# Kernel optimization log

Hardware: AMD Instinct MI355X
Metric: run time of the kernel (lower is better)

## Reference

```python
import jax, jax.numpy as jnp
import numpy as np

N = 16384          # total nodes (128 graphs x 128 ops)
G = 128            # number of graphs
NPG = N // G       # nodes per graph
DIN = 64           # op_input_dim
H = 64             # hidden_dim
BN_EPS = 1e-5


def setup_inputs() -> dict:
    key = jax.random.key(0)
    ks = jax.random.split(key, 16)
    x = jax.random.normal(ks[0], (N, DIN), dtype=jnp.float32)
    # sparse-ish 0/1 adjacency stored dense (as torch.mm path expects); add self-loops so degrees > 0
    u = jax.random.uniform(ks[1], (N, N), dtype=jnp.float32)
    adj = jnp.maximum((u < 0.004).astype(jnp.float32), jnp.eye(N, dtype=jnp.float32))
    # graph_pool: [G, N] average-pooling matrix (block rows of 1/NPG)
    rows = jnp.repeat(jnp.arange(G), NPG)
    graph_pool = jnp.zeros((G, N), jnp.float32).at[rows, jnp.arange(N)].set(1.0 / NPG)
    s = 0.05
    params = {}
    dims_in = [DIN, H]
    for l in range(2):
        d_in = dims_in[l]
        params[f"W1_{l}"] = jax.random.normal(ks[2 + 6 * l], (d_in, H), jnp.float32) * s
        params[f"b1_{l}"] = jnp.zeros((H,), jnp.float32)
        params[f"g1_{l}"] = jnp.ones((H,), jnp.float32)
        params[f"be1_{l}"] = jnp.zeros((H,), jnp.float32)
        params[f"W2_{l}"] = jax.random.normal(ks[3 + 6 * l], (H, H), jnp.float32) * s
        params[f"b2_{l}"] = jnp.zeros((H,), jnp.float32)
        params[f"g_{l}"] = jnp.ones((H,), jnp.float32)   # outer BN gamma
        params[f"be_{l}"] = jnp.zeros((H,), jnp.float32)  # outer BN beta
    return {"x": x, "adj": adj, "graph_pool": graph_pool, **params}


def _bn(h, g, b):
    # training-mode BatchNorm1d over node axis (biased var), eps=1e-5
    m = jnp.mean(h, axis=0)
    v = jnp.var(h, axis=0)
    return g * (h - m) * jax.lax.rsqrt(v + BN_EPS) + b


def _mlp(h, W1, b1, g1, be1, W2, b2):
    # 2-layer MLP: Linear -> BN -> ReLU -> Linear
    return jax.nn.relu(_bn(h @ W1 + b1, g1, be1)) @ W2 + b2


def reference(x, adj, graph_pool,
              W1_0, b1_0, g1_0, be1_0, W2_0, b2_0, g_0, be_0,
              W1_1, b1_1, g1_1, be1_1, W2_1, b2_1, g_1, be_1):
    deg = adj @ jnp.ones((adj.shape[0], 1), adj.dtype)  # [N,1]
    h = x
    layers = [
        (W1_0, b1_0, g1_0, be1_0, W2_0, b2_0, g_0, be_0),
        (W1_1, b1_1, g1_1, be1_1, W2_1, b2_1, g_1, be_1),
    ]
    for (W1, b1, g1, be1, W2, b2, g, be) in layers:
        pooled = (adj @ h) / deg                 # average neighbor aggregation
        pooled_rep = _mlp(pooled, W1, b1, g1, be1, W2, b2)
        h = jax.nn.relu(_bn(pooled_rep, g, be))
    h_nodes = h
    pooled_h = graph_pool @ h                    # [G, H] graph readout
    return (pooled_h, h_nodes)
```

## Files before the change

### kernel.cpp

```cpp
#include <hip/hip_runtime.h>
#include <hip/hip_bf16.h>
#include <stdint.h>

#define N_NODES 16384
#define GG      128
#define HD      64
#define MAXD    192
#define BN_EPS  1e-5f
#define NSLOT   16

typedef unsigned short u16;
typedef unsigned int   u32;
typedef unsigned long long u64;
typedef u32 u32x4 __attribute__((ext_vector_type(4)));

__device__ __forceinline__ float bf2f(u16 u) {
    union { u32 i; float f; } c; c.i = ((u32)u) << 16; return c.f;
}
__device__ __forceinline__ float ldp(const void* p, int i, int flag) {
    return flag ? ((const float*)p)[i] : bf2f(((const u16*)p)[i]);
}

__global__ __launch_bounds__(256) void k_scan_gather(
    const void* __restrict__ adjv, const void* __restrict__ xv,
    u16* __restrict__ cols, int* __restrict__ cnt,
    float* __restrict__ invdeg, float* __restrict__ pooled,
    double* __restrict__ statsD, int* __restrict__ flagp)
{
    __shared__ __align__(16) u16 sc[4][MAXD];
    const int wave = threadIdx.x >> 6, lane = threadIdx.x & 63;
    const int row = blockIdx.x * 4 + wave;
    const u32 w0 = *(const u32*)adjv;
    const int flag = ((w0 & 0xFFFFu) == 0) ? 1 : 0;
    const u64 ltmask = ((1ull << lane) - 1ull);

    const int gid = blockIdx.x * 256 + threadIdx.x;
    if (gid < 4 * NSLOT * 128) statsD[gid] = 0.0;
    if (gid == 0) *flagp = flag;

    u16* __restrict__ srow = sc[wave];
    int base = 0;
    if (flag) {
        const u32x4* __restrict__ arow =
            (const u32x4*)((const u32*)adjv + (size_t)row * N_NODES) + lane;
        u32x4 p0 = __builtin_nontemporal_load(arow);
        u32x4 p1 = __builtin_nontemporal_load(arow + 64);
        for (int c = 0; c < N_NODES; c += 256) {
            u32x4 raw = p0;
            p0 = p1;
            if (c + 512 < N_NODES)
                p1 = __builtin_nontemporal_load(arow + (c + 512) / 4);
            #pragma unroll
            for (int e = 0; e < 4; ++e) {
                u32 w = raw[e];
                u64 m = __ballot(w != 0);
                if (m) {
                    if (w) {
                        int p = base + __popcll(m & ltmask);
                        if (p < MAXD) srow[p] = (u16)(c + lane * 4 + e);
                    }
                    base += __popcll(m);
                }
            }
        }
    } else {
        const u32x4* __restrict__ arow =
            (const u32x4*)((const u16*)adjv + (size_t)row * N_NODES) + lane;
        u32x4 p0 = __builtin_nontemporal_load(arow);
        u32x4 p1 = __builtin_nontemporal_load(arow + 64);
        for (int c = 0; c < N_NODES; c += 512) {
            u32x4 raw = p0;
            p0 = p1;
            if (c + 1024 < N_NODES)
                p1 = __builtin_nontemporal_load(arow + (c + 1024) / 8);
            #pragma unroll
            for (int e = 0; e < 8; ++e) {
                u16 u = (u16)(raw[e >> 1] >> ((e & 1) * 16));
                u64 m = __ballot(u != 0);
                if (m) {
                    if (u) {
                        int p = base + __popcll(m & ltmask);
                        if (p < MAXD) srow[p] = (u16)(c + lane * 8 + e);
                    }
                    base += __popcll(m);
                }
            }
        }
    }
    const int n = (base < MAXD) ? base : MAXD;
    if (lane == 0) cnt[row] = n;
    __syncthreads();

    {
        u32* __restrict__ crow32 = (u32*)(cols + (size_t)row * MAXD);
        const u32* __restrict__ s32 = (const u32*)srow;
        #pragma unroll
        for (int t = lane; t < MAXD / 2; t += 64) crow32[t] = s32[t];
    }

    float acc = 0.f;
    int k = 0;
    if (flag) {
        const float* __restrict__ x = (const float*)xv;
        for (; k + 4 <= n; k += 4) {
            ushort4 j4 = *(const ushort4*)&srow[k];
            float v0 = x[(size_t)j4.x * HD + lane];
            float v1 = x[(size_t)j4.y * HD + lane];
            float v2 = x[(size_t)j4.z * HD + lane];
            float v3 = x[(size_t)j4.w * HD + lane];
            acc += (v0 + v1) + (v2 + v3);
        }
        for (; k < n; ++k) acc += x[(size_t)srow[k] * HD + lane];
    } else {
        const u16* __restrict__ x = (const u16*)xv;
        for (; k + 4 <= n; k += 4) {
            ushort4 j4 = *(const ushort4*)&srow[k];
            float v0 = bf2f(x[(size_t)j4.x * HD + lane]);
            float v1 = bf2f(x[(size_t)j4.y * HD + lane]);
            float v2 = bf2f(x[(size_t)j4.z * HD + lane]);
            float v3 = bf2f(x[(size_t)j4.w * HD + lane]);
            acc += (v0 + v1) + (v2 + v3);
        }
        for (; k < n; ++k) acc += bf2f(x[(size_t)srow[k] * HD + lane]);
    }
    float inv = 1.f / (float)n;
    pooled[(size_t)row * HD + lane] = acc * inv;
    if (lane == 0) invdeg[row] = inv;
}

template<bool AFFINE>
__global__ __launch_bounds__(256) void k_mm(
    const float* __restrict__ src, const double* __restrict__ statsIn,
    const void* __restrict__ g, const void* __restrict__ be,
    const void* __restrict__ W, const void* __restrict__ bias,
    float* __restrict__ dst, double* __restrict__ statsOut,
    const int* __restrict__ flagp)
{
    __shared__ float Wf[64 * 64];
    __shared__ float S[16 * 64];
    __shared__ float ac[128];
    __shared__ double shs[256];
    __shared__ double shq[256];
    const int tid = threadIdx.x;
    const int flag = *flagp;
    if (AFFINE) {
        if (tid < 64) {
            double ss = 0.0, qq = 0.0;
            #pragma unroll
            for (int s2 = 0; s2 < NSLOT; ++s2) {
                ss += statsIn[s2 * 128 + tid];
                qq += statsIn[s2 * 128 + 64 + tid];
            }
            double m = ss * (1.0 / N_NODES);
            double v = qq * (1.0 / N_NODES) - m * m;
            float A = ldp(g, tid, flag) / sqrtf((float)v + BN_EPS);
            ac[tid] = A;
            ac[64 + tid] = ldp(be, tid, flag) - (float)m * A;
        }
        __syncthreads();
    }
    for (int i = tid; i < 64 * 64; i += 256) Wf[i] = ldp(W, i, flag);
    const int rbase = blockIdx.x * 16;
    {
        float4 v = *(const float4*)&src[(size_t)rbase * 64 + tid * 4];
        if (AFFINE) {
            const int f0 = (tid * 4) & 63;
            v.x = fmaxf(fmaf(ac[f0 + 0], v.x, ac[64 + f0 + 0]), 0.f);
            v.y = fmaxf(fmaf(ac[f0 + 1], v.y, ac[64 + f0 + 1]), 0.f);
            v.z = fmaxf(fmaf(ac[f0 + 2], v.z, ac[64 + f0 + 2]), 0.f);
            v.w = fmaxf(fmaf(ac[f0 + 3], v.w, ac[64 + f0 + 3]), 0.f);
        }
        *(float4*)&S[tid * 4] = v;
    }
    __syncthreads();
    const int f = tid & 63, r0 = (tid >> 6) * 4;
    const float b = ldp(bias, f, flag);
    float a0 = b, a1 = b, a2 = b, a3 = b;
    #pragma unroll
    for (int k = 0; k < 64; ++k) {
        const float wk = Wf[k * 64 + f];
        a0 = fmaf(S[(r0 + 0) * 64 + k], wk, a0);
        a1 = fmaf(S[(r0 + 1) * 64 + k], wk, a1);
        a2 = fmaf(S[(r0 + 2) * 64 + k], wk, a2);
        a3 = fmaf(S[(r0 + 3) * 64 + k], wk, a3);
    }
    dst[(size_t)(rbase + r0 + 0) * 64 + f] = a0;
    dst[(size_t)(rbase + r0 + 1) * 64 + f] = a1;
    dst[(size_t)(rbase + r0 + 2) * 64 + f] = a2;
    dst[(size_t)(rbase + r0 + 3) * 64 + f] = a3;

    shs[tid] = (double)a0 + (double)a1 + (double)a2 + (double)a3;
    shq[tid] = (double)a0 * a0 + (double)a1 * a1
             + (double)a2 * a2 + (double)a3 * a3;
    __syncthreads();
    if (tid < 64) {
        double S2 = shs[tid] + shs[64 + tid] + shs[128 + tid] + shs[192 + tid];
        double Q2 = shq[tid] + shq[64 + tid] + shq[128 + tid] + shq[192 + tid];
        double* so = statsOut + (blockIdx.x & (NSLOT - 1)) * 128;
        atomicAdd(&so[tid], S2);
        atomicAdd(&so[64 + tid], Q2);
    }
}

__global__ __launch_bounds__(256) void k_spmm(
    const float* __restrict__ t, const double* __restrict__ statsIn,
    const void* __restrict__ g, const void* __restrict__ be,
    const u16* __restrict__ cols, const int* __restrict__ cnt,
    const float* __restrict__ invdeg, float* __restrict__ pooled,
    const int* __restrict__ flagp)
{
    __shared__ float ac[128];
    const int tid = threadIdx.x;
    const int wave = tid >> 6, lane = tid & 63;
    const int row = blockIdx.x * 4 + wave;
    const int flag = *flagp;
    if (tid < 64) {
        double ss = 0.0, qq = 0.0;
        #pragma unroll
        for (int s2 = 0; s2 < NSLOT; ++s2) {
            ss += statsIn[s2 * 128 + tid];
            qq += statsIn[s2 * 128 + 64 + tid];
        }
        double m = ss * (1.0 / N_NODES);
        double v = qq * (1.0 / N_NODES) - m * m;
        float A = ldp(g, tid, flag) / sqrtf((float)v + BN_EPS);
        ac[tid] = A;
        ac[64 + tid] = ldp(be, tid, flag) - (float)m * A;
    }
    __syncthreads();
    const float A = ac[lane], C = ac[64 + lane];

    const u16* __restrict__ crow = cols + (size_t)row * MAXD;
    const int n = cnt[row];
    float acc = 0.f;
    int k = 0;
    for (; k + 4 <= n; k += 4) {
        ushort4 j4 = *(const ushort4*)&crow[k];
        float v0 = t[(size_t)j4.x * HD + lane];
        float v1 = t[(size_t)j4.y * HD + lane];
        float v2 = t[(size_t)j4.z * HD + lane];
        float v3 = t[(size_t)j4.w * HD + lane];
        acc += fmaxf(fmaf(A, v0, C), 0.f);
        acc += fmaxf(fmaf(A, v1, C), 0.f);
        acc += fmaxf(fmaf(A, v2, C), 0.f);
        acc += fmaxf(fmaf(A, v3, C), 0.f);
    }
    for (; k < n; ++k) {
        float vv = t[(size_t)crow[k] * HD + lane];
        acc += fmaxf(fmaf(A, vv, C), 0.f);
    }
    pooled[(size_t)row * HD + lane] = acc * invdeg[row];
}

__global__ __launch_bounds__(1024) void k_bnrelu_pool(
    const float* __restrict__ P, const double* __restrict__ statsIn,
    const void* __restrict__ g, const void* __restrict__ be,
    const void* __restrict__ gpv, float* __restrict__ out_nodes,
    float* __restrict__ out_pool, const int* __restrict__ flagp)
{
    __shared__ float ac[128];
    __shared__ float red[16 * 64];
    const int tid = threadIdx.x;
    const int flag = *flagp;
    if (tid < 64) {
        double ss = 0.0, qq = 0.0;
        #pragma unroll
        for (int s2 = 0; s2 < NSLOT; ++s2) {
            ss += statsIn[s2 * 128 + tid];
            qq += statsIn[s2 * 128 + 64 + tid];
        }
        double m = ss * (1.0 / N_NODES);
        double v = qq * (1.0 / N_NODES) - m * m;
        float A = ldp(g, tid, flag) / sqrtf((float)v + BN_EPS);
        ac[tid] = A;
        ac[64 + tid] = ldp(be, tid, flag) - (float)m * A;
    }
    __syncthreads();

    if (blockIdx.x < 256) {
        const size_t idx = ((size_t)blockIdx.x * 1024 + tid) * 4;
        const int f0 = (int)(idx & 63);
        float4 t = *(const float4*)&P[idx];
        const float4 A4 = *(const float4*)&ac[f0];
        const float4 C4 = *(const float4*)&ac[64 + f0];
        float4 r;
        r.x = fmaxf(fmaf(A4.x, t.x, C4.x), 0.f);
        r.y = fmaxf(fmaf(A4.y, t.y, C4.y), 0.f);
        r.z = fmaxf(fmaf(A4.z, t.z, C4.z), 0.f);
        r.w = fmaxf(fmaf(A4.w, t.w, C4.w), 0.f);
        *(float4*)&out_nodes[idx] = r;
    } else {
        const int gidx = blockIdx.x - 256;
        const int wave = tid >> 6, lane = tid & 63;
        const float A = ac[lane], C = ac[64 + lane];
        float acc = 0.f;
        const int jb0 = wave * (N_NODES / 16);
        if (flag) {
            const float* __restrict__ grow =
                (const float*)gpv + (size_t)gidx * N_NODES;
            for (int jb = jb0; jb < jb0 + N_NODES / 16; jb += 4) {
                float4 raw = *(const float4*)(grow + jb);
                if (raw.x != 0.f)
                    acc += raw.x * fmaxf(fmaf(A, P[(size_t)(jb + 0) * HD + lane], C), 0.f);
                if (raw.y != 0.f)
                    acc += raw.y * fmaxf(fmaf(A, P[(size_t)(jb + 1) * HD + lane], C), 0.f);
                if (raw.z != 0.f)
                    acc += raw.z * fmaxf(fmaf(A, P[(size_t)(jb + 2) * HD + lane], C), 0.f);
                if (raw.w != 0.f)
                    acc += raw.w * fmaxf(fmaf(A, P[(size_t)(jb + 3) * HD + lane], C), 0.f);
            }
        } else {
            const u16* __restrict__ grow =
                (const u16*)gpv + (size_t)gidx * N_NODES;
            for (int jb = jb0; jb < jb0 + N_NODES / 16; jb += 8) {
                uint4 raw = *(const uint4*)(grow + jb);
                const u32 w[4] = {raw.x, raw.y, raw.z, raw.w};
                #pragma unroll
                for (int e = 0; e < 8; ++e) {
                    u16 u = (u16)(w[e >> 1] >> ((e & 1) * 16));
                    if (u)
                        acc += bf2f(u) * fmaxf(fmaf(A, P[(size_t)(jb + e) * HD + lane], C), 0.f);
                }
            }
        }
        red[wave * 64 + lane] = acc;
        __syncthreads();
        if (wave == 0) {
            float s = 0.f;
            #pragma unroll
            for (int w2 = 0; w2 < 16; ++w2) s += red[w2 * 64 + lane];
            out_pool[gidx * 64 + lane] = s;
        }
    }
}

extern "C" void kernel_launch(void* const* d_in, const int* in_sizes, int n_in,
                              void* d_out, int out_size, void* d_ws, size_t ws_size,
                              hipStream_t stream)
{
    const void* x    = d_in[0];
    const void* adj  = d_in[1];
    const void* gp   = d_in[2];
    const void* W1_0 = d_in[3];
    const void* b1_0 = d_in[4];
    const void* g1_0 = d_in[5];
    const void* be1_0= d_in[6];
    const void* W2_0 = d_in[7];
    const void* b2_0 = d_in[8];
    const void* g_0  = d_in[9];
    const void* be_0 = d_in[10];
    const void* W1_1 = d_in[11];
    const void* b1_1 = d_in[12];
    const void* g1_1 = d_in[13];
    const void* be1_1= d_in[14];
    const void* W2_1 = d_in[15];
    const void* b2_1 = d_in[16];
    const void* g_1  = d_in[17];
    const void* be_1 = d_in[18];

    char* ws = (char*)d_ws;
    float*  P      = (float*) (ws);
    float*  A      = (float*) (ws + (4u  << 20));
    float*  B      = (float*) (ws + (8u  << 20));
    u16*    cols   = (u16*)   (ws + (12u << 20));
    int*    cnt    = (int*)   (ws + (18u << 20));
    float*  invdeg = (float*) (ws + (18u << 20) + 65536);
    double* sd     = (double*)(ws + (18u << 20) + 131072);
    int*    flag   = (int*)   (ws + (18u << 20) + 131072 + 65536);

    float* out_pool  = (float*)d_out;
    float* out_nodes = (float*)d_out + GG * HD;

    double* st0 = sd + 0 * NSLOT * 128;
    double* st1 = sd + 1 * NSLOT * 128;
    double* st2 = sd + 2 * NSLOT * 128;
    double* st3 = sd + 3 * NSLOT * 128;

    k_scan_gather<<<N_NODES / 4, 256, 0, stream>>>(adj, x, cols, cnt,
                                                   invdeg, P, sd, flag);

    k_mm<false><<<N_NODES / 16, 256, 0, stream>>>(P, nullptr, nullptr, nullptr,
                                                  W1_0, b1_0, A, st0, flag);
    k_mm<true><<<N_NODES / 16, 256, 0, stream>>>(A, st0, g1_0, be1_0,
                                                 W2_0, b2_0, P, st1, flag);
    k_spmm<<<N_NODES / 4, 256, 0, stream>>>(P, st1, g_0, be_0,
                                            cols, cnt, invdeg, B, flag);
    k_mm<false><<<N_NODES / 16, 256, 0, stream>>>(B, nullptr, nullptr, nullptr,
                                                  W1_1, b1_1, A, st2, flag);
    k_mm<true><<<N_NODES / 16, 256, 0, stream>>>(A, st2, g1_1, be1_1,
                                                 W2_1, b2_1, P, st3, flag);
    k_bnrelu_pool<<<256 + GG, 1024, 0, stream>>>(P, st3, g_1, be_1, gp,
                                                 out_nodes, out_pool, flag);
}
```

Baseline: 1.544 ms.

## Fuse post-scan stages into one persistent kernel with atomic grid barriers

Replaces the six kernels after the adjacency scan (two MLP matmuls per layer, the sparse aggregation, BN/ReLU and pooling) with one 1024-block persistent kernel. Grid-wide atomic barriers separate the BatchNorm statistics phases. Matmul results stay in registers and LDS across phases, so several global round trips and launch gaps go away. The risk is a deadlock if all 1024 blocks cannot be resident at once, plus barrier spin overhead; the graph pooling now uses only 128 blocks of 4 waves each.

```diff
diff --git a/kernel.cpp b/kernel.cpp
--- a/kernel.cpp
+++ b/kernel.cpp
@@ -8,6 +8,8 @@
 #define MAXD    192
 #define BN_EPS  1e-5f
 #define NSLOT   16
+#define STG     (NSLOT * 128)
+#define NBLK    1024
 
 typedef unsigned short u16;
 typedef unsigned int   u32;
@@ -25,7 +27,8 @@
     const void* __restrict__ adjv, const void* __restrict__ xv,
     u16* __restrict__ cols, int* __restrict__ cnt,
     float* __restrict__ invdeg, float* __restrict__ pooled,
-    double* __restrict__ statsD, int* __restrict__ flagp)
+    double* __restrict__ statsD, int* __restrict__ barp,
+    int* __restrict__ flagp)
 {
     __shared__ __align__(16) u16 sc[4][MAXD];
     const int wave = threadIdx.x >> 6, lane = threadIdx.x & 63;
@@ -35,7 +38,8 @@
     const u64 ltmask = ((1ull << lane) - 1ull);
 
     const int gid = blockIdx.x * 256 + threadIdx.x;
-    if (gid < 4 * NSLOT * 128) statsD[gid] = 0.0;
+    if (gid < 4 * STG) statsD[gid] = 0.0;
+    if (gid < 8) barp[gid] = 0;
     if (gid == 0) *flagp = flag;
 
     u16* __restrict__ srow = sc[wave];
@@ -128,28 +132,58 @@
     if (lane == 0) invdeg[row] = inv;
 }
 
-template<bool AFFINE>
-__global__ __launch_bounds__(256) void k_mm(
-    const float* __restrict__ src, const double* __restrict__ statsIn,
-    const void* __restrict__ g, const void* __restrict__ be,
-    const void* __restrict__ W, const void* __restrict__ bias,
-    float* __restrict__ dst, double* __restrict__ statsOut,
+__global__ __launch_bounds__(256, 4) void k_fused(
+    const float* __restrict__ P0, const u16* __restrict__ cols,
+    const int* __restrict__ cnt, const float* __restrict__ invdeg,
+    float* __restrict__ H0, float* __restrict__ H1,
+    double* __restrict__ sd, int* __restrict__ bar,
+    const void* __restrict__ gpv,
+    const void* __restrict__ W1_0, const void* __restrict__ b1_0,
+    const void* __restrict__ g1_0, const void* __restrict__ be1_0,
+    const void* __restrict__ W2_0, const void* __restrict__ b2_0,
+    const void* __restrict__ g_0,  const void* __restrict__ be_0,
+    const void* __restrict__ W1_1, const void* __restrict__ b1_1,
+    const void* __restrict__ g1_1, const void* __restrict__ be1_1,
+    const void* __restrict__ W2_1, const void* __restrict__ b2_1,
+    const void* __restrict__ g_1,  const void* __restrict__ be_1,
+    float* __restrict__ out_nodes, float* __restrict__ out_pool,
     const int* __restrict__ flagp)
 {
-    __shared__ float Wf[64 * 64];
-    __shared__ float S[16 * 64];
-    __shared__ float ac[128];
+    __shared__ float  Wf[64 * 64];
+    __shared__ float  S[16 * 64];
+    __shared__ float  ac[128];
     __shared__ double shs[256];
     __shared__ double shq[256];
-    const int tid = threadIdx.x;
+    __shared__ float  red[4 * 64];
+
+    const int tid  = threadIdx.x;
     const int flag = *flagp;
-    if (AFFINE) {
+    const int rbase = blockIdx.x * 16;
+    const int f = tid & 63, r0 = (tid >> 6) * 4;
+    const int wave = tid >> 6, lane = tid & 63;
+
+    auto gridbar = [&](int idx) {
+        __syncthreads();
+        if (tid == 0) {
+            __threadfence();
+            __hip_atomic_fetch_add(&bar[idx], 1, __ATOMIC_ACQ_REL,
+                                   __HIP_MEMORY_SCOPE_AGENT);
+            while (__hip_atomic_load(&bar[idx], __ATOMIC_ACQUIRE,
+                                     __HIP_MEMORY_SCOPE_AGENT) < NBLK)
+                __builtin_amdgcn_s_sleep(8);
+        }
+        __syncthreads();
+    };
+    auto stageW = [&](const void* W) {
+        for (int i = tid; i < 64 * 64; i += 256) Wf[i] = ldp(W, i, flag);
+    };
+    auto mkac = [&](const double* st, const void* g, const void* be) {
         if (tid < 64) {
             double ss = 0.0, qq = 0.0;
             #pragma unroll
             for (int s2 = 0; s2 < NSLOT; ++s2) {
-                ss += statsIn[s2 * 128 + tid];
-                qq += statsIn[s2 * 128 + 64 + tid];
+                ss += st[s2 * 128 + tid];
+                qq += st[s2 * 128 + 64 + tid];
             }
             double m = ss * (1.0 / N_NODES);
             double v = qq * (1.0 / N_NODES) - m * m;
@@ -157,179 +191,159 @@
             ac[tid] = A;
             ac[64 + tid] = ldp(be, tid, flag) - (float)m * A;
         }
+    };
+    auto mm = [&](const void* bias, float& a0, float& a1, float& a2, float& a3) {
+        const float b = ldp(bias, f, flag);
+        a0 = b; a1 = b; a2 = b; a3 = b;
+        #pragma unroll
+        for (int k = 0; k < 64; ++k) {
+            const float wk = Wf[k * 64 + f];
+            a0 = fmaf(S[(r0 + 0) * 64 + k], wk, a0);
+            a1 = fmaf(S[(r0 + 1) * 64 + k], wk, a1);
+            a2 = fmaf(S[(r0 + 2) * 64 + k], wk, a2);
+            a3 = fmaf(S[(r0 + 3) * 64 + k], wk, a3);
+        }
+    };
+    auto stats = [&](double* st, float a0, float a1, float a2, float a3) {
+        shs[tid] = (double)a0 + (double)a1 + (double)a2 + (double)a3;
+        shq[tid] = (double)a0 * a0 + (double)a1 * a1
+                 + (double)a2 * a2 + (double)a3 * a3;
         __syncthreads();
-    }
-    for (int i = tid; i < 64 * 64; i += 256) Wf[i] = ldp(W, i, flag);
-    const int rbase = blockIdx.x * 16;
+        if (tid < 64) {
+            double S2 = shs[tid] + shs[64 + tid] + shs[128 + tid] + shs[192 + tid];
+            double Q2 = shq[tid] + shq[64 + tid] + shq[128 + tid] + shq[192 + tid];
+            double* so = st + (blockIdx.x & (NSLOT - 1)) * 128;
+            atomicAdd(&so[tid], S2);
+            atomicAdd(&so[64 + tid], Q2);
+        }
+    };
+    auto affine_to_S = [&](float a0, float a1, float a2, float a3) {
+        const float A = ac[f], C = ac[64 + f];
+        S[(r0 + 0) * 64 + f] = fmaxf(fmaf(A, a0, C), 0.f);
+        S[(r0 + 1) * 64 + f] = fmaxf(fmaf(A, a1, C), 0.f);
+        S[(r0 + 2) * 64 + f] = fmaxf(fmaf(A, a2, C), 0.f);
+        S[(r0 + 3) * 64 + f] = fmaxf(fmaf(A, a3, C), 0.f);
+    };
+
+    float a0, a1, a2, a3;
+
+    stageW(W1_0);
     {
-        float4 v = *(const float4*)&src[(size_t)rbase * 64 + tid * 4];
-        if (AFFINE) {
-            const int f0 = (tid * 4) & 63;
-            v.x = fmaxf(fmaf(ac[f0 + 0], v.x, ac[64 + f0 + 0]), 0.f);
-            v.y = fmaxf(fmaf(ac[f0 + 1], v.y, ac[64 + f0 + 1]), 0.f);
-            v.z = fmaxf(fmaf(ac[f0 + 2], v.z, ac[64 + f0 + 2]), 0.f);
-            v.w = fmaxf(fmaf(ac[f0 + 3], v.w, ac[64 + f0 + 3]), 0.f);
-        }
+        float4 v = *(const float4*)&P0[(size_t)rbase * 64 + tid * 4];
         *(float4*)&S[tid * 4] = v;
     }
     __syncthreads();
-    const int f = tid & 63, r0 = (tid >> 6) * 4;
-    const float b = ldp(bias, f, flag);
-    float a0 = b, a1 = b, a2 = b, a3 = b;
-    #pragma unroll
-    for (int k = 0; k < 64; ++k) {
-        const float wk = Wf[k * 64 + f];
-        a0 = fmaf(S[(r0 + 0) * 64 + k], wk, a0);
-        a1 = fmaf(S[(r0 + 1) * 64 + k], wk, a1);
-        a2 = fmaf(S[(r0 + 2) * 64 + k], wk, a2);
-        a3 = fmaf(S[(r0 + 3) * 64 + k], wk, a3);
-    }
-    dst[(size_t)(rbase + r0 + 0) * 64 + f] = a0;
-    dst[(size_t)(rbase + r0 + 1) * 64 + f] = a1;
-    dst[(size_t)(rbase + r0 + 2) * 64 + f] = a2;
-    dst[(size_t)(rbase + r0 + 3) * 64 + f] = a3;
-
-    shs[tid] = (double)a0 + (double)a1 + (double)a2 + (double)a3;
-    shq[tid] = (double)a0 * a0 + (double)a1 * a1
-             + (double)a2 * a2 + (double)a3 * a3;
-    __syncthreads();
-    if (tid < 64) {
-        double S2 = shs[tid] + shs[64 + tid] + shs[128 + tid] + shs[192 + tid];
-        double Q2 = shq[tid] + shq[64 + tid] + shq[128 + tid] + shq[192 + tid];
-        double* so = statsOut + (blockIdx.x & (NSLOT - 1)) * 128;
-        atomicAdd(&so[tid], S2);
-        atomicAdd(&so[64 + tid], Q2);
-    }
-}
-
-__global__ __launch_bounds__(256) void k_spmm(
-    const float* __restrict__ t, const double* __restrict__ statsIn,
-    const void* __restrict__ g, const void* __restrict__ be,
-    const u16* __restrict__ cols, const int* __restrict__ cnt,
-    const float* __restrict__ invdeg, float* __restrict__ pooled,
-    const int* __restrict__ flagp)
-{
-    __shared__ float ac[128];
-    const int tid = threadIdx.x;
-    const int wave = tid >> 6, lane = tid & 63;
-    const int row = blockIdx.x * 4 + wave;
-    const int flag = *flagp;
-    if (tid < 64) {
-        double ss = 0.0, qq = 0.0;
-        #pragma unroll
-        for (int s2 = 0; s2 < NSLOT; ++s2) {
-            ss += statsIn[s2 * 128 + tid];
-            qq += statsIn[s2 * 128 + 64 + tid];
-        }
-        double m = ss * (1.0 / N_NODES);
-        double v = qq * (1.0 / N_NODES) - m * m;
-        float A = ldp(g, tid, flag) / sqrtf((float)v + BN_EPS);
-        ac[tid] = A;
-        ac[64 + tid] = ldp(be, tid, flag) - (float)m * A;
-    }
-    __syncthreads();
-    const float A = ac[lane], C = ac[64 + lane];
-
-    const u16* __restrict__ crow = cols + (size_t)row * MAXD;
-    const int n = cnt[row];
-    float acc = 0.f;
-    int k = 0;
-    for (; k + 4 <= n; k += 4) {
-        ushort4 j4 = *(const ushort4*)&crow[k];
-        float v0 = t[(size_t)j4.x * HD + lane];
-        float v1 = t[(size_t)j4.y * HD + lane];
-        float v2 = t[(size_t)j4.z * HD + lane];
-        float v3 = t[(size_t)j4.w * HD + lane];
-        acc += fmaxf(fmaf(A, v0, C), 0.f);
-        acc += fmaxf(fmaf(A, v1, C), 0.f);
-        acc += fmaxf(fmaf(A, v2, C), 0.f);
-        acc += fmaxf(fmaf(A, v3, C), 0.f);
-    }
-    for (; k < n; ++k) {
-        float vv = t[(size_t)crow[k] * HD + lane];
-        acc += fmaxf(fmaf(A, vv, C), 0.f);
-    }
-    pooled[(size_t)row * HD + lane] = acc * invdeg[row];
-}
-
-__global__ __launch_bounds__(1024) void k_bnrelu_pool(
-    const float* __restrict__ P, const double* __restrict__ statsIn,
-    const void* __restrict__ g, const void* __restrict__ be,
-    const void* __restrict__ gpv, float* __restrict__ out_nodes,
-    float* __restrict__ out_pool, const int* __restrict__ flagp)
-{
-    __shared__ float ac[128];
-    __shared__ float red[16 * 64];
-    const int tid = threadIdx.x;
-    const int flag = *flagp;
-    if (tid < 64) {
-        double ss = 0.0, qq = 0.0;
-        #pragma unroll
-        for (int s2 = 0; s2 < NSLOT; ++s2) {
-            ss += statsIn[s2 * 128 + tid];
-            qq += statsIn[s2 * 128 + 64 + tid];
-        }
-        double m = ss * (1.0 / N_NODES);
-        double v = qq * (1.0 / N_NODES) - m * m;
-        float A = ldp(g, tid, flag) / sqrtf((float)v + BN_EPS);
-        ac[tid] = A;
-        ac[64 + tid] = ldp(be, tid, flag) - (float)m * A;
-    }
-    __syncthreads();
-
-    if (blockIdx.x < 256) {
-        const size_t idx = ((size_t)blockIdx.x * 1024 + tid) * 4;
-        const int f0 = (int)(idx & 63);
-        float4 t = *(const float4*)&P[idx];
-        const float4 A4 = *(const float4*)&ac[f0];
-        const float4 C4 = *(const float4*)&ac[64 + f0];
-        float4 r;
-        r.x = fmaxf(fmaf(A4.x, t.x, C4.x), 0.f);
-        r.y = fmaxf(fmaf(A4.y, t.y, C4.y), 0.f);
-        r.z = fmaxf(fmaf(A4.z, t.z, C4.z), 0.f);
-        r.w = fmaxf(fmaf(A4.w, t.w, C4.w), 0.f);
-        *(float4*)&out_nodes[idx] = r;
-    } else {
-        const int gidx = blockIdx.x - 256;
-        const int wave = tid >> 6, lane = tid & 63;
+    mm(b1_0, a0, a1, a2, a3);
+    stats(sd + 0 * STG, a0, a1, a2, a3);
+    gridbar(0);
+
+    mkac(sd + 0 * STG, g1_0, be1_0);
+    stageW(W2_0);
+    __syncthreads();
+    affine_to_S(a0, a1, a2, a3);
+    __syncthreads();
+    mm(b2_0, a0, a1, a2, a3);
+    H0[(size_t)(rbase + r0 + 0) * 64 + f] = a0;
+    H0[(size_t)(rbase + r0 + 1) * 64 + f] = a1;
+    H0[(size_t)(rbase + r0 + 2) * 64 + f] = a2;
+    H0[(size_t)(rbase + r0 + 3) * 64 + f] = a3;
+    stats(sd + 1 * STG, a0, a1, a2, a3);
+    gridbar(1);
+
+    mkac(sd + 1 * STG, g_0, be_0);
+    stageW(W1_1);
+    __syncthreads();
+    {
+        const float A = ac[lane], C = ac[64 + lane];
+        for (int ri = 0; ri < 4; ++ri) {
+            const int row = rbase + wave * 4 + ri;
+            const u16* __restrict__ crow = cols + (size_t)row * MAXD;
+            const int n = cnt[row];
+            float acc = 0.f;
+            int k = 0;
+            for (; k + 4 <= n; k += 4) {
+                ushort4 j4 = *(const ushort4*)&crow[k];
+                float v0 = H0[(size_t)j4.x * HD + lane];
+                float v1 = H0[(size_t)j4.y * HD + lane];
+                float v2 = H0[(size_t)j4.z * HD + lane];
+                float v3 = H0[(size_t)j4.w * HD + lane];
+                acc += fmaxf(fmaf(A, v0, C), 0.f);
+                acc += fmaxf(fmaf(A, v1, C), 0.f);
+                acc += fmaxf(fmaf(A, v2, C), 0.f);
+                acc += fmaxf(fmaf(A, v3, C), 0.f);
+            }
+            for (; k < n; ++k) {
+                float vv = H0[(size_t)crow[k] * HD + lane];
+                acc += fmaxf(fmaf(A, vv, C), 0.f);
+            }
+            S[(wave * 4 + ri) * 64 + lane] = acc * invdeg[row];
+        }
+    }
+    __syncthreads();
+    mm(b1_1, a0, a1, a2, a3);
+    stats(sd + 2 * STG, a0, a1, a2, a3);
+    gridbar(2);
+
+    mkac(sd + 2 * STG, g1_1, be1_1);
+    stageW(W2_1);
+    __syncthreads();
+    affine_to_S(a0, a1, a2, a3);
+    __syncthreads();
+    mm(b2_1, a0, a1, a2, a3);
+    H1[(size_t)(rbase + r0 + 0) * 64 + f] = a0;
+    H1[(size_t)(rbase + r0 + 1) * 64 + f] = a1;
+    H1[(size_t)(rbase + r0 + 2) * 64 + f] = a2;
+    H1[(size_t)(rbase + r0 + 3) * 64 + f] = a3;
+    stats(sd + 3 * STG, a0, a1, a2, a3);
+    gridbar(3);
+
+    mkac(sd + 3 * STG, g_1, be_1);
+    __syncthreads();
+    {
+        const float A = ac[f], C = ac[64 + f];
+        out_nodes[(size_t)(rbase + r0 + 0) * 64 + f] = fmaxf(fmaf(A, a0, C), 0.f);
+        out_nodes[(size_t)(rbase + r0 + 1) * 64 + f] = fmaxf(fmaf(A, a1, C), 0.f);
+        out_nodes[(size_t)(rbase + r0 + 2) * 64 + f] = fmaxf(fmaf(A, a2, C), 0.f);
+        out_nodes[(size_t)(rbase + r0 + 3) * 64 + f] = fmaxf(fmaf(A, a3, C), 0.f);
+    }
+    if (blockIdx.x < GG) {
+        const int g = blockIdx.x;
         const float A = ac[lane], C = ac[64 + lane];
         float acc = 0.f;
-        const int jb0 = wave * (N_NODES / 16);
+        const int jb0 = wave * (N_NODES / 4);
         if (flag) {
             const float* __restrict__ grow =
-                (const float*)gpv + (size_t)gidx * N_NODES;
-            for (int jb = jb0; jb < jb0 + N_NODES / 16; jb += 4) {
+                (const float*)gpv + (size_t)g * N_NODES;
+            for (int jb = jb0; jb < jb0 + N_NODES / 4; jb += 4) {
                 float4 raw = *(const float4*)(grow + jb);
                 if (raw.x != 0.f)
-                    acc += raw.x * fmaxf(fmaf(A, P[(size_t)(jb + 0) * HD + lane], C), 0.f);
+                    acc += raw.x * fmaxf(fmaf(A, H1[(size_t)(jb + 0) * HD + lane], C), 0.f);
                 if (raw.y != 0.f)
-                    acc += raw.y * fmaxf(fmaf(A, P[(size_t)(jb + 1) * HD + lane], C), 0.f);
+                    acc += raw.y * fmaxf(fmaf(A, H1[(size_t)(jb + 1) * HD + lane], C), 0.f);
                 if (raw.z != 0.f)
-                    acc += raw.z * fmaxf(fmaf(A, P[(size_t)(jb + 2) * HD + lane], C), 0.f);
+                    acc += raw.z * fmaxf(fmaf(A, H1[(size_t)(jb + 2) * HD + lane], C), 0.f);
                 if (raw.w != 0.f)
-                    acc += raw.w * fmaxf(fmaf(A, P[(size_t)(jb + 3) * HD + lane], C), 0.f);
+                    acc += raw.w * fmaxf(fmaf(A, H1[(size_t)(jb + 3) * HD + lane], C), 0.f);
             }
         } else {
             const u16* __restrict__ grow =
-                (const u16*)gpv + (size_t)gidx * N_NODES;
-            for (int jb = jb0; jb < jb0 + N_NODES / 16; jb += 8) {
+                (const u16*)gpv + (size_t)g * N_NODES;
+            for (int jb = jb0; jb < jb0 + N_NODES / 4; jb += 8) {
                 uint4 raw = *(const uint4*)(grow + jb);
                 const u32 w[4] = {raw.x, raw.y, raw.z, raw.w};
                 #pragma unroll
                 for (int e = 0; e < 8; ++e) {
                     u16 u = (u16)(w[e >> 1] >> ((e & 1) * 16));
                     if (u)
-                        acc += bf2f(u) * fmaxf(fmaf(A, P[(size_t)(jb + e) * HD + lane], C), 0.f);
+                        acc += bf2f(u) * fmaxf(fmaf(A, H1[(size_t)(jb + e) * HD + lane], C), 0.f);
                 }
             }
         }
         red[wave * 64 + lane] = acc;
         __syncthreads();
         if (wave == 0) {
-            float s = 0.f;
-            #pragma unroll
-            for (int w2 = 0; w2 < 16; ++w2) s += red[w2 * 64 + lane];
-            out_pool[gidx * 64 + lane] = s;
+            float s = red[lane] + red[64 + lane] + red[128 + lane] + red[192 + lane];
+            out_pool[g * 64 + lane] = s;
         }
     }
 }
@@ -359,36 +373,27 @@
     const void* be_1 = d_in[18];
 
     char* ws = (char*)d_ws;
-    float*  P      = (float*) (ws);
-    float*  A      = (float*) (ws + (4u  << 20));
-    float*  B      = (float*) (ws + (8u  << 20));
+    float*  P0     = (float*) (ws);
+    float*  H0     = (float*) (ws + (4u  << 20));
+    float*  H1     = (float*) (ws + (8u  << 20));
     u16*    cols   = (u16*)   (ws + (12u << 20));
     int*    cnt    = (int*)   (ws + (18u << 20));
     float*  invdeg = (float*) (ws + (18u << 20) + 65536);
     double* sd     = (double*)(ws + (18u << 20) + 131072);
-    int*    flag   = (int*)   (ws + (18u << 20) + 131072 + 65536);
+    int*    flag   = (int*)   (ws + (18u << 20) + 196608);
+    int*    bar    = (int*)   (ws + (18u << 20) + 196608 + 64);
 
     float* out_pool  = (float*)d_out;
     float* out_nodes = (float*)d_out + GG * HD;
 
-    double* st0 = sd + 0 * NSLOT * 128;
-    double* st1 = sd + 1 * NSLOT * 128;
-    double* st2 = sd + 2 * NSLOT * 128;
-    double* st3 = sd + 3 * NSLOT * 128;
-
     k_scan_gather<<<N_NODES / 4, 256, 0, stream>>>(adj, x, cols, cnt,
-                                                   invdeg, P, sd, flag);
-
-    k_mm<false><<<N_NODES / 16, 256, 0, stream>>>(P, nullptr, nullptr, nullptr,
-                                                  W1_0, b1_0, A, st0, flag);
-    k_mm<true><<<N_NODES / 16, 256, 0, stream>>>(A, st0, g1_0, be1_0,
-                                                 W2_0, b2_0, P, st1, flag);
-    k_spmm<<<N_NODES / 4, 256, 0, stream>>>(P, st1, g_0, be_0,
-                                            cols, cnt, invdeg, B, flag);
-    k_mm<false><<<N_NODES / 16, 256, 0, stream>>>(B, nullptr, nullptr, nullptr,
-                                                  W1_1, b1_1, A, st2, flag);
-    k_mm<true><<<N_NODES / 16, 256, 0, stream>>>(A, st2, g1_1, be1_1,
-                                                 W2_1, b2_1, P, st3, flag);
-    k_bnrelu_pool<<<256 + GG, 1024, 0, stream>>>(P, st3, g_1, be_1, gp,
-                                                 out_nodes, out_pool, flag);
-}
+                                                   invdeg, P0, sd, bar, flag);
+
+    k_fused<<<NBLK, 256, 0, stream>>>(P0, cols, cnt, invdeg, H0, H1, sd, bar,
+                                      gp,
+                                      W1_0, b1_0, g1_0, be1_0, W2_0, b2_0,
+                                      g_0, be_0,
+                                      W1_1, b1_1, g1_1, be1_1, W2_1, b2_1,
+                                      g_1, be_1,
+                                      out_nodes, out_pool, flag);
+}
```

New measurement: 2.071 ms. +34.2%, slower.

## Fuse first linear layer into scan-gather and SpMM aggregation kernels

Applied to the files above, without the earlier changes.

Fuses the first MLP linear (W1 plus bias, with BatchNorm stats accumulation) of each layer into the preceding aggregation kernel. Layer 0 does it in the adjacency scan/gather kernel and layer 1 in the SpMM kernel, which now handles 16 rows per block. This removes two kernel launches and the write and re-read of the pooled intermediate. The cost is more shared memory per block. The scan kernel also loads the 16KB W tile in every one of its 4096 blocks, and the SpMM kernel has fewer blocks with more serial gather work per wave.

```diff
diff --git a/kernel.cpp b/kernel.cpp
--- a/kernel.cpp
+++ b/kernel.cpp
@@ -8,6 +8,7 @@
 #define MAXD    192
 #define BN_EPS  1e-5f
 #define NSLOT   16
+#define STG     (NSLOT * 128)
 
 typedef unsigned short u16;
 typedef unsigned int   u32;
@@ -21,22 +22,31 @@
     return flag ? ((const float*)p)[i] : bf2f(((const u16*)p)[i]);
 }
 
-__global__ __launch_bounds__(256) void k_scan_gather(
+__global__ __launch_bounds__(256) void k_scan_gather_mm(
     const void* __restrict__ adjv, const void* __restrict__ xv,
     u16* __restrict__ cols, int* __restrict__ cnt,
-    float* __restrict__ invdeg, float* __restrict__ pooled,
-    double* __restrict__ statsD, int* __restrict__ flagp)
+    float* __restrict__ invdeg,
+    const void* __restrict__ W, const void* __restrict__ bias,
+    float* __restrict__ dstA, double* __restrict__ statsOut,
+    double* __restrict__ statsArena, int* __restrict__ flagp)
 {
+    __shared__ float  Wf[64 * 64];
     __shared__ __align__(16) u16 sc[4][MAXD];
-    const int wave = threadIdx.x >> 6, lane = threadIdx.x & 63;
-    const int row = blockIdx.x * 4 + wave;
+    __shared__ float  S[4 * 64];
+    __shared__ double shs[256];
+    __shared__ double shq[256];
+    const int tid  = threadIdx.x;
+    const int wave = tid >> 6, lane = tid & 63;
+    const int row  = blockIdx.x * 4 + wave;
     const u32 w0 = *(const u32*)adjv;
     const int flag = ((w0 & 0xFFFFu) == 0) ? 1 : 0;
     const u64 ltmask = ((1ull << lane) - 1ull);
 
-    const int gid = blockIdx.x * 256 + threadIdx.x;
-    if (gid < 4 * NSLOT * 128) statsD[gid] = 0.0;
+    const int gid = blockIdx.x * 256 + tid;
+    if (gid < 4 * STG) statsArena[gid] = 0.0;
     if (gid == 0) *flagp = flag;
+
+    for (int i = tid; i < 64 * 64; i += 256) Wf[i] = ldp(W, i, flag);
 
     u16* __restrict__ srow = sc[wave];
     int base = 0;
@@ -124,12 +134,30 @@
         for (; k < n; ++k) acc += bf2f(x[(size_t)srow[k] * HD + lane]);
     }
     float inv = 1.f / (float)n;
-    pooled[(size_t)row * HD + lane] = acc * inv;
+    S[wave * 64 + lane] = acc * inv;
     if (lane == 0) invdeg[row] = inv;
-}
-
-template<bool AFFINE>
-__global__ __launch_bounds__(256) void k_mm(
+    __syncthreads();
+
+    const int f = tid & 63, r = tid >> 6;
+    float a = ldp(bias, f, flag);
+    #pragma unroll
+    for (int kk = 0; kk < 64; ++kk)
+        a = fmaf(S[r * 64 + kk], Wf[kk * 64 + f], a);
+    dstA[(size_t)(blockIdx.x * 4 + r) * 64 + f] = a;
+
+    shs[tid] = (double)a;
+    shq[tid] = (double)a * a;
+    __syncthreads();
+    if (tid < 64) {
+        double S2 = shs[tid] + shs[64 + tid] + shs[128 + tid] + shs[192 + tid];
+        double Q2 = shq[tid] + shq[64 + tid] + shq[128 + tid] + shq[192 + tid];
+        double* so = statsOut + (blockIdx.x & (NSLOT - 1)) * 128;
+        atomicAdd(&so[tid], S2);
+        atomicAdd(&so[64 + tid], Q2);
+    }
+}
+
+__global__ __launch_bounds__(256) void k_mm_affine(
     const float* __restrict__ src, const double* __restrict__ statsIn,
     const void* __restrict__ g, const void* __restrict__ be,
     const void* __restrict__ W, const void* __restrict__ bias,
@@ -143,33 +171,29 @@
     __shared__ double shq[256];
     const int tid = threadIdx.x;
     const int flag = *flagp;
-    if (AFFINE) {
-        if (tid < 64) {
-            double ss = 0.0, qq = 0.0;
-            #pragma unroll
-            for (int s2 = 0; s2 < NSLOT; ++s2) {
-                ss += statsIn[s2 * 128 + tid];
-                qq += statsIn[s2 * 128 + 64 + tid];
-            }
-            double m = ss * (1.0 / N_NODES);
-            double v = qq * (1.0 / N_NODES) - m * m;
-            float A = ldp(g, tid, flag) / sqrtf((float)v + BN_EPS);
-            ac[tid] = A;
-            ac[64 + tid] = ldp(be, tid, flag) - (float)m * A;
-        }
-        __syncthreads();
+    if (tid < 64) {
+        double ss = 0.0, qq = 0.0;
+        #pragma unroll
+        for (int s2 = 0; s2 < NSLOT; ++s2) {
+            ss += statsIn[s2 * 128 + tid];
+            qq += statsIn[s2 * 128 + 64 + tid];
+        }
+        double m = ss * (1.0 / N_NODES);
+        double v = qq * (1.0 / N_NODES) - m * m;
+        float A = ldp(g, tid, flag) / sqrtf((float)v + BN_EPS);
+        ac[tid] = A;
+        ac[64 + tid] = ldp(be, tid, flag) - (float)m * A;
     }
     for (int i = tid; i < 64 * 64; i += 256) Wf[i] = ldp(W, i, flag);
+    __syncthreads();
     const int rbase = blockIdx.x * 16;
     {
         float4 v = *(const float4*)&src[(size_t)rbase * 64 + tid * 4];
-        if (AFFINE) {
-            const int f0 = (tid * 4) & 63;
-            v.x = fmaxf(fmaf(ac[f0 + 0], v.x, ac[64 + f0 + 0]), 0.f);
-            v.y = fmaxf(fmaf(ac[f0 + 1], v.y, ac[64 + f0 + 1]), 0.f);
-            v.z = fmaxf(fmaf(ac[f0 + 2], v.z, ac[64 + f0 + 2]), 0.f);
-            v.w = fmaxf(fmaf(ac[f0 + 3], v.w, ac[64 + f0 + 3]), 0.f);
-        }
+        const int f0 = (tid * 4) & 63;
+        v.x = fmaxf(fmaf(ac[f0 + 0], v.x, ac[64 + f0 + 0]), 0.f);
+        v.y = fmaxf(fmaf(ac[f0 + 1], v.y, ac[64 + f0 + 1]), 0.f);
+        v.z = fmaxf(fmaf(ac[f0 + 2], v.z, ac[64 + f0 + 2]), 0.f);
+        v.w = fmaxf(fmaf(ac[f0 + 3], v.w, ac[64 + f0 + 3]), 0.f);
         *(float4*)&S[tid * 4] = v;
     }
     __syncthreads();
@@ -202,17 +226,22 @@
     }
 }
 
-__global__ __launch_bounds__(256) void k_spmm(
+__global__ __launch_bounds__(256) void k_spmm_mm(
     const float* __restrict__ t, const double* __restrict__ statsIn,
     const void* __restrict__ g, const void* __restrict__ be,
     const u16* __restrict__ cols, const int* __restrict__ cnt,
-    const float* __restrict__ invdeg, float* __restrict__ pooled,
+    const float* __restrict__ invdeg,
+    const void* __restrict__ W, const void* __restrict__ bias,
+    float* __restrict__ dstA, double* __restrict__ statsOut,
     const int* __restrict__ flagp)
 {
+    __shared__ float Wf[64 * 64];
+    __shared__ float S[16 * 64];
     __shared__ float ac[128];
+    __shared__ double shs[256];
+    __shared__ double shq[256];
     const int tid = threadIdx.x;
     const int wave = tid >> 6, lane = tid & 63;
-    const int row = blockIdx.x * 4 + wave;
     const int flag = *flagp;
     if (tid < 64) {
         double ss = 0.0, qq = 0.0;
@@ -227,29 +256,65 @@
         ac[tid] = A;
         ac[64 + tid] = ldp(be, tid, flag) - (float)m * A;
     }
-    __syncthreads();
-    const float A = ac[lane], C = ac[64 + lane];
-
-    const u16* __restrict__ crow = cols + (size_t)row * MAXD;
-    const int n = cnt[row];
-    float acc = 0.f;
-    int k = 0;
-    for (; k + 4 <= n; k += 4) {
-        ushort4 j4 = *(const ushort4*)&crow[k];
-        float v0 = t[(size_t)j4.x * HD + lane];
-        float v1 = t[(size_t)j4.y * HD + lane];
-        float v2 = t[(size_t)j4.z * HD + lane];
-        float v3 = t[(size_t)j4.w * HD + lane];
-        acc += fmaxf(fmaf(A, v0, C), 0.f);
-        acc += fmaxf(fmaf(A, v1, C), 0.f);
-        acc += fmaxf(fmaf(A, v2, C), 0.f);
-        acc += fmaxf(fmaf(A, v3, C), 0.f);
-    }
-    for (; k < n; ++k) {
-        float vv = t[(size_t)crow[k] * HD + lane];
-        acc += fmaxf(fmaf(A, vv, C), 0.f);
-    }
-    pooled[(size_t)row * HD + lane] = acc * invdeg[row];
+    for (int i = tid; i < 64 * 64; i += 256) Wf[i] = ldp(W, i, flag);
+    __syncthreads();
+
+    const int rbase = blockIdx.x * 16;
+    {
+        const float A = ac[lane], C = ac[64 + lane];
+        for (int ri = 0; ri < 4; ++ri) {
+            const int row = rbase + wave * 4 + ri;
+            const u16* __restrict__ crow = cols + (size_t)row * MAXD;
+            const int n = cnt[row];
+            float acc = 0.f;
+            int k = 0;
+            for (; k + 4 <= n; k += 4) {
+                ushort4 j4 = *(const ushort4*)&crow[k];
+                float v0 = t[(size_t)j4.x * HD + lane];
+                float v1 = t[(size_t)j4.y * HD + lane];
+                float v2 = t[(size_t)j4.z * HD + lane];
+                float v3 = t[(size_t)j4.w * HD + lane];
+                acc += fmaxf(fmaf(A, v0, C), 0.f);
+                acc += fmaxf(fmaf(A, v1, C), 0.f);
+                acc += fmaxf(fmaf(A, v2, C), 0.f);
+                acc += fmaxf(fmaf(A, v3, C), 0.f);
+            }
+            for (; k < n; ++k) {
+                float vv = t[(size_t)crow[k] * HD + lane];
+                acc += fmaxf(fmaf(A, vv, C), 0.f);
+            }
+            S[(wave * 4 + ri) * 64 + lane] = acc * invdeg[row];
+        }
+    }
+    __syncthreads();
+
+    const int f = tid & 63, r0 = (tid >> 6) * 4;
+    const float b = ldp(bias, f, flag);
+    float a0 = b, a1 = b, a2 = b, a3 = b;
+    #pragma unroll
+    for (int k = 0; k < 64; ++k) {
+        const float wk = Wf[k * 64 + f];
+        a0 = fmaf(S[(r0 + 0) * 64 + k], wk, a0);
+        a1 = fmaf(S[(r0 + 1) * 64 + k], wk, a1);
+        a2 = fmaf(S[(r0 + 2) * 64 + k], wk, a2);
+        a3 = fmaf(S[(r0 + 3) * 64 + k], wk, a3);
+    }
+    dstA[(size_t)(rbase + r0 + 0) * 64 + f] = a0;
+    dstA[(size_t)(rbase + r0 + 1) * 64 + f] = a1;
+    dstA[(size_t)(rbase + r0 + 2) * 64 + f] = a2;
+    dstA[(size_t)(rbase + r0 + 3) * 64 + f] = a3;
+
+    shs[tid] = (double)a0 + (double)a1 + (double)a2 + (double)a3;
+    shq[tid] = (double)a0 * a0 + (double)a1 * a1
+             + (double)a2 * a2 + (double)a3 * a3;
+    __syncthreads();
+    if (tid < 64) {
+        double S2 = shs[tid] + shs[64 + tid] + shs[128 + tid] + shs[192 + tid];
+        double Q2 = shq[tid] + shq[64 + tid] + shq[128 + tid] + shq[192 + tid];
+        double* so = statsOut + (blockIdx.x & (NSLOT - 1)) * 128;
+        atomicAdd(&so[tid], S2);
+        atomicAdd(&so[64 + tid], Q2);
+    }
 }
 
 __global__ __launch_bounds__(1024) void k_bnrelu_pool(
@@ -359,36 +424,31 @@
     const void* be_1 = d_in[18];
 
     char* ws = (char*)d_ws;
-    float*  P      = (float*) (ws);
-    float*  A      = (float*) (ws + (4u  << 20));
-    float*  B      = (float*) (ws + (8u  << 20));
+    float*  Abuf   = (float*) (ws);
+    float*  H0     = (float*) (ws + (4u  << 20));
+    float*  H1     = (float*) (ws + (8u  << 20));
     u16*    cols   = (u16*)   (ws + (12u << 20));
     int*    cnt    = (int*)   (ws + (18u << 20));
     float*  invdeg = (float*) (ws + (18u << 20) + 65536);
     double* sd     = (double*)(ws + (18u << 20) + 131072);
-    int*    flag   = (int*)   (ws + (18u << 20) + 131072 + 65536);
+    int*    flag   = (int*)   (ws + (18u << 20) + 196608);
 
     float* out_pool  = (float*)d_out;
     float* out_nodes = (float*)d_out + GG * HD;
 
-    double* st0 = sd + 0 * NSLOT * 128;
-    double* st1 = sd + 1 * NSLOT * 128;
-    double* st2 = sd + 2 * NSLOT * 128;
-    double* st3 = sd + 3 * NSLOT * 128;
-
-    k_scan_gather<<<N_NODES / 4, 256, 0, stream>>>(adj, x, cols, cnt,
-                                                   invdeg, P, sd, flag);
-
-    k_mm<false><<<N_NODES / 16, 256, 0, stream>>>(P, nullptr, nullptr, nullptr,
-                                                  W1_0, b1_0, A, st0, flag);
-    k_mm<true><<<N_NODES / 16, 256, 0, stream>>>(A, st0, g1_0, be1_0,
-                                                 W2_0, b2_0, P, st1, flag);
-    k_spmm<<<N_NODES / 4, 256, 0, stream>>>(P, st1, g_0, be_0,
-                                            cols, cnt, invdeg, B, flag);
-    k_mm<false><<<N_NODES / 16, 256, 0, stream>>>(B, nullptr, nullptr, nullptr,
-                                                  W1_1, b1_1, A, st2, flag);
-    k_mm<true><<<N_NODES / 16, 256, 0, stream>>>(A, st2, g1_1, be1_1,
-                                                 W2_1, b2_1, P, st3, flag);
-    k_bnrelu_pool<<<256 + GG, 1024, 0, stream>>>(P, st3, g_1, be_1, gp,
-                                                 out_nodes, out_pool, flag);
-}
+    double* st0 = sd + 0 * STG;
+    double* st1 = sd + 1 * STG;
+    double* st2 = sd + 2 * STG;
+    double* st3 = sd + 3 * STG;
+
+    k_scan_gather_mm<<<N_NODES / 4, 256, 0, stream>>>(
+        adj, x, cols, cnt, invdeg, W1_0, b1_0, Abuf, st0, sd, flag);
+    k_mm_affine<<<N_NODES / 16, 256, 0, stream>>>(
+        Abuf, st0, g1_0, be1_0, W2_0, b2_0, H0, st1, flag);
+    k_spmm_mm<<<N_NODES / 16, 256, 0, stream>>>(
+        H0, st1, g_0, be_0, cols, cnt, invdeg, W1_1, b1_1, Abuf, st2, flag);
+    k_mm_affine<<<N_NODES / 16, 256, 0, stream>>>(
+        Abuf, st2, g1_1, be1_1, W2_1, b2_1, H1, st3, flag);
+    k_bnrelu_pool<<<256 + GG, 1024, 0, stream>>>(
+        H1, st3, g_1, be_1, gp, out_nodes, out_pool, flag);
+}
```

Result: no change. 1.565 ms (+1.4%).
